# Performance work log

Measured on AMD Instinct MI355X. Metric: run time of the kernel, lower is better.

The kernel has to match this reference:

```python
import jax, jax.numpy as jnp
import numpy as np

NUM_HEADS = 8
Q_DIM = 32  # == k_dim == v_dim (required by the broadcasted matmul in the source)

def _conv1x1(x, w, b):
    # x: [B, C, H, W]; w: [O, C]; b: [O]  (1x1 conv == channel matmul)
    return jnp.einsum('bchw,oc->bohw', x, w) + b[None, :, None, None]

def setup_inputs() -> dict:
    key = jax.random.key(0)
    ks = jax.random.split(key, 7)
    B, C, H, W = 16, 256, 64, 64
    O = Q_DIM * NUM_HEADS  # 256
    s = 1.0 / np.sqrt(C)
    return {
        'x':  jax.random.normal(ks[0], (B, C, H, W), jnp.float32),
        'wq': jax.random.normal(ks[1], (O, C), jnp.float32) * s,
        'bq': jax.random.normal(ks[2], (O,), jnp.float32) * 0.01,
        'wk': jax.random.normal(ks[3], (O, C), jnp.float32) * s,
        'bk': jax.random.normal(ks[4], (O,), jnp.float32) * 0.01,
        'wv': jax.random.normal(ks[5], (O, C), jnp.float32) * s,
        'bv': jax.random.normal(ks[6], (O,), jnp.float32) * 0.01,
    }

def reference(x, wq, bq, wk, bk, wv, bv):
    B, C, H, W = x.shape
    nH, d = NUM_HEADS, Q_DIM
    q = _conv1x1(x, wq, bq).reshape(B, nH, d, H, W)
    k = _conv1x1(x, wk, bk).reshape(B, nH, d, H, W)
    v = _conv1x1(x, wv, bv).reshape(B, nH, d, H, W)
    # torch.matmul(q, k.transpose(-2,-1)): contract over width, batched over (B, nH, d)
    scores = jnp.einsum('bndhw,bndgw->bndhg', q, k) / jnp.sqrt(jnp.asarray(d, x.dtype))
    weights = jax.nn.softmax(scores, axis=-1)  # [B, nH, d, H, H]
    ctx = jnp.einsum('bndhg,bndgw->bndhw', weights, v)
    return ctx.reshape(B, nH * d, H, W)
```

## Files before the change

kernel.cpp:

```cpp
#include <hip/hip_runtime.h>
#include <stdint.h>

#define LOG2E       1.4426950408889634f
#define INV_SQRT32  0.17677669529663687f

using bf16x8 = __attribute__((ext_vector_type(8))) short;
using f32x4  = __attribute__((ext_vector_type(4))) float;

__device__ __forceinline__ unsigned short f2bf(float f) {
  union { float f; uint32_t u; } v; v.f = f;
  uint32_t r = v.u + 0x7fffu + ((v.u >> 16) & 1u);
  return (unsigned short)(r >> 16);
}

typedef const __attribute__((address_space(1))) void* gas_ptr;
typedef __attribute__((address_space(3))) void*       las_ptr;
__device__ __forceinline__ void load_lds16(const void* g, void* l) {
  __builtin_amdgcn_global_load_lds((gas_ptr)g, (las_ptr)l, 16, 0, 0);
}

__global__ __launch_bounds__(256) void convert_w(
    const float* __restrict__ wq, const float* __restrict__ bq,
    const float* __restrict__ wk, const float* __restrict__ bk,
    const float* __restrict__ wv, const float* __restrict__ bv,
    unsigned short* __restrict__ Wcat, float* __restrict__ biasc) {
  int idx = (blockIdx.x * 256 + threadIdx.x) * 4;
  int p = idx >> 16;
  int rem = idx & 0xffff;
  const float* src = (p == 0) ? wq : (p == 1) ? wk : wv;
  float4 v = *(const float4*)(src + rem);
  ushort4 o;
  o.x = f2bf(v.x); o.y = f2bf(v.y); o.z = f2bf(v.z); o.w = f2bf(v.w);
  *(ushort4*)(Wcat + idx) = o;
  if (blockIdx.x < 3) {
    const float* sb = (blockIdx.x == 0) ? bq : (blockIdx.x == 1) ? bk : bv;
    biasc[blockIdx.x * 256 + threadIdx.x] = sb[threadIdx.x];
  }
}

__global__ __launch_bounds__(256) void transpose_x(const float* __restrict__ x,
                                                   unsigned short* __restrict__ xt) {
  __shared__ float tile[64 * 65];
  int b = blockIdx.z;
  int s0 = blockIdx.x * 64, c0 = blockIdx.y * 64;
  int t = threadIdx.x;
  int sl = t & 63, g = t >> 6;
  const float* xp = x + ((size_t)(b * 256 + c0)) * 4096 + s0 + sl;
#pragma unroll
  for (int ii = 0; ii < 16; ++ii) {
    int cl = g * 16 + ii;
    tile[cl * 65 + sl] = xp[(size_t)cl * 4096];
  }
  __syncthreads();
#pragma unroll
  for (int jj = 0; jj < 16; ++jj) {
    int s_loc = g * 16 + jj;
    float v = tile[sl * 65 + s_loc];
    xt[((size_t)(b * 4096 + s0 + s_loc)) * 256 + c0 + sl] = f2bf(v);
  }
}

__global__ __launch_bounds__(256) void gemm_qkv(
    const unsigned short* __restrict__ Wc, const float* __restrict__ biasc,
    const unsigned short* __restrict__ Xt, unsigned short* __restrict__ qkv) {
  __shared__ unsigned short As[128 * 32];
  __shared__ unsigned short Bs[128 * 32];
  int blk = blockIdx.x;
  int b = blk / 192;
  int rest = blk - b * 192;
  int mt = rest >> 5, nt = rest & 31;
  int m0 = mt * 128, n0 = nt * 128;
  int tid = threadIdx.x;
  int lane = tid & 63, wave = tid >> 6;
  int quad = lane >> 4, rt = lane & 15;
  int wm = wave >> 1, wn = wave & 1;

  f32x4 acc[4][4];
#pragma unroll
  for (int i = 0; i < 4; ++i)
#pragma unroll
    for (int j = 0; j < 4; ++j) acc[i][j] = (f32x4){0.f, 0.f, 0.f, 0.f};

  int lr = lane >> 2;
  int lk = (lane & 3) * 8;
  const unsigned short* gA0 = Wc + (size_t)(m0 + (wave * 2 + 0) * 16 + lr) * 256 + lk;
  const unsigned short* gA1 = Wc + (size_t)(m0 + (wave * 2 + 1) * 16 + lr) * 256 + lk;
  const unsigned short* gB0 = Xt + ((size_t)b * 4096 + n0 + (wave * 2 + 0) * 16 + lr) * 256 + lk;
  const unsigned short* gB1 = Xt + ((size_t)b * 4096 + n0 + (wave * 2 + 1) * 16 + lr) * 256 + lk;
  unsigned short* lA0 = &As[(wave * 2 + 0) * 16 * 32];
  unsigned short* lA1 = &As[(wave * 2 + 1) * 16 * 32];
  unsigned short* lB0 = &Bs[(wave * 2 + 0) * 16 * 32];
  unsigned short* lB1 = &Bs[(wave * 2 + 1) * 16 * 32];

#pragma unroll
  for (int kc = 0; kc < 8; ++kc) {
    int ko = kc * 32;
    load_lds16(gA0 + ko, lA0);
    load_lds16(gA1 + ko, lA1);
    load_lds16(gB0 + ko, lB0);
    load_lds16(gB1 + ko, lB1);
    __syncthreads();
    bf16x8 af[4], bfr[4];
#pragma unroll
    for (int mi = 0; mi < 4; ++mi)
      af[mi] = *(const bf16x8*)&As[(wm * 64 + mi * 16 + rt) * 32 + quad * 8];
#pragma unroll
    for (int ni = 0; ni < 4; ++ni)
      bfr[ni] = *(const bf16x8*)&Bs[(wn * 64 + ni * 16 + rt) * 32 + quad * 8];
#pragma unroll
    for (int mi = 0; mi < 4; ++mi)
#pragma unroll
      for (int ni = 0; ni < 4; ++ni)
        acc[mi][ni] = __builtin_amdgcn_mfma_f32_16x16x32_bf16(af[mi], bfr[ni], acc[mi][ni], 0, 0, 0);
    __syncthreads();
  }

  size_t obase = (size_t)b * 768;
#pragma unroll
  for (int mi = 0; mi < 4; ++mi) {
    int o = m0 + wm * 64 + mi * 16 + quad * 4;
    float bsv[4];
#pragma unroll
    for (int r = 0; r < 4; ++r) bsv[r] = biasc[o + r];
#pragma unroll
    for (int ni = 0; ni < 4; ++ni) {
      int s = n0 + wn * 64 + ni * 16 + rt;
#pragma unroll
      for (int r = 0; r < 4; ++r)
        qkv[(obase + o + r) * 4096 + s] = f2bf(acc[mi][ni][r] + bsv[r]);
    }
  }
}

__global__ __launch_bounds__(256) void attn(const unsigned short* __restrict__ qkv,
                                            float* __restrict__ out) {
  __shared__ char sh[36608];
  unsigned short* Qs = (unsigned short*)sh;
  unsigned short* Ks = (unsigned short*)(sh + 9216);
  float*          Sf = (float*)sh;
  unsigned short* Ps = (unsigned short*)(sh + 16640);
  unsigned short* Vt = (unsigned short*)(sh + 25856);
  float* red    = (float*)(sh + 35072);
  float* rowmax = (float*)(sh + 36096);
  float* rowinv = (float*)(sh + 36352);

  int blk = blockIdx.x;
  int b = blk >> 8, o = blk & 255;
  int t = threadIdx.x;
  size_t base = ((size_t)b * 768 + o) * 4096;
  const unsigned short* qg = qkv + base;
  const unsigned short* kg = qkv + base + (size_t)256 * 4096;
  const unsigned short* vg = qkv + base + (size_t)512 * 4096;

  {
    int h = t >> 2, w0 = (t & 3) * 16;
    const uint4* qp = (const uint4*)(qg + h * 64 + w0);
    const uint4* kp = (const uint4*)(kg + h * 64 + w0);
    uint4 q0 = qp[0], q1 = qp[1];
    uint4 k0 = kp[0], k1 = kp[1];
    *(uint4*)&Qs[h * 72 + w0]     = q0;
    *(uint4*)&Qs[h * 72 + w0 + 8] = q1;
    *(uint4*)&Ks[h * 72 + w0]     = k0;
    *(uint4*)&Ks[h * 72 + w0 + 8] = k1;

    int w = t & 63, gb = (t >> 6) * 16;
    unsigned short vv[16];
#pragma unroll
    for (int j = 0; j < 16; ++j) vv[j] = vg[(size_t)(gb + j) * 64 + w];
    *(uint4*)&Vt[w * 72 + gb]     = ((uint4*)vv)[0];
    *(uint4*)&Vt[w * 72 + gb + 8] = ((uint4*)vv)[1];
  }
  __syncthreads();

  int lane = t & 63, wave = t >> 6;
  int rt = lane & 15, quad = lane >> 4;
  int wm = wave >> 1, wn = wave & 1;

  f32x4 accs[2][2];
#pragma unroll
  for (int i = 0; i < 2; ++i)
#pragma unroll
    for (int j = 0; j < 2; ++j) accs[i][j] = (f32x4){0.f, 0.f, 0.f, 0.f};
#pragma unroll
  for (int ks = 0; ks < 2; ++ks) {
    int kk = ks * 32 + quad * 8;
    bf16x8 a0 = *(const bf16x8*)&Qs[(wm * 32 + rt) * 72 + kk];
    bf16x8 a1 = *(const bf16x8*)&Qs[(wm * 32 + 16 + rt) * 72 + kk];
    bf16x8 b0 = *(const bf16x8*)&Ks[(wn * 32 + rt) * 72 + kk];
    bf16x8 b1 = *(const bf16x8*)&Ks[(wn * 32 + 16 + rt) * 72 + kk];
    accs[0][0] = __builtin_amdgcn_mfma_f32_16x16x32_bf16(a0, b0, accs[0][0], 0, 0, 0);
    accs[0][1] = __builtin_amdgcn_mfma_f32_16x16x32_bf16(a0, b1, accs[0][1], 0, 0, 0);
    accs[1][0] = __builtin_amdgcn_mfma_f32_16x16x32_bf16(a1, b0, accs[1][0], 0, 0, 0);
    accs[1][1] = __builtin_amdgcn_mfma_f32_16x16x32_bf16(a1, b1, accs[1][1], 0, 0, 0);
  }
  __syncthreads();

#pragma unroll
  for (int tm = 0; tm < 2; ++tm)
#pragma unroll
    for (int tn = 0; tn < 2; ++tn)
#pragma unroll
      for (int r = 0; r < 4; ++r)
        Sf[(wm * 32 + tm * 16 + quad * 4 + r) * 65 + wn * 32 + tn * 16 + rt] =
            accs[tm][tn][r] * INV_SQRT32;
  __syncthreads();

  int hr = t & 63, qt = t >> 6;
  float s[16];
#pragma unroll
  for (int e = 0; e < 16; ++e) s[e] = Sf[hr * 65 + qt * 16 + e];
  float m = s[0];
#pragma unroll
  for (int e = 1; e < 16; ++e) m = fmaxf(m, s[e]);
  red[qt * 64 + hr] = m;
  __syncthreads();
  if (t < 64)
    rowmax[t] = fmaxf(fmaxf(red[t], red[64 + t]), fmaxf(red[128 + t], red[192 + t]));
  __syncthreads();
  float mr = rowmax[hr];
  float ssum = 0.f;
  unsigned short pv[16];
#pragma unroll
  for (int e = 0; e < 16; ++e) {
    float p = exp2f((s[e] - mr) * LOG2E);
    ssum += p;
    pv[e] = f2bf(p);
  }
  *(uint4*)&Ps[hr * 72 + qt * 16]     = ((uint4*)pv)[0];
  *(uint4*)&Ps[hr * 72 + qt * 16 + 8] = ((uint4*)pv)[1];
  red[qt * 64 + hr] = ssum;
  __syncthreads();
  if (t < 64) rowinv[t] = 1.f / (red[t] + red[64 + t] + red[128 + t] + red[192 + t]);
  __syncthreads();

  f32x4 acco[2][2];
#pragma unroll
  for (int i = 0; i < 2; ++i)
#pragma unroll
    for (int j = 0; j < 2; ++j) acco[i][j] = (f32x4){0.f, 0.f, 0.f, 0.f};
#pragma unroll
  for (int ks = 0; ks < 2; ++ks) {
    int kk = ks * 32 + quad * 8;
    bf16x8 a0 = *(const bf16x8*)&Ps[(wm * 32 + rt) * 72 + kk];
    bf16x8 a1 = *(const bf16x8*)&Ps[(wm * 32 + 16 + rt) * 72 + kk];
    bf16x8 b0 = *(const bf16x8*)&Vt[(wn * 32 + rt) * 72 + kk];
    bf16x8 b1 = *(const bf16x8*)&Vt[(wn * 32 + 16 + rt) * 72 + kk];
    acco[0][0] = __builtin_amdgcn_mfma_f32_16x16x32_bf16(a0, b0, acco[0][0], 0, 0, 0);
    acco[0][1] = __builtin_amdgcn_mfma_f32_16x16x32_bf16(a0, b1, acco[0][1], 0, 0, 0);
    acco[1][0] = __builtin_amdgcn_mfma_f32_16x16x32_bf16(a1, b0, acco[1][0], 0, 0, 0);
    acco[1][1] = __builtin_amdgcn_mfma_f32_16x16x32_bf16(a1, b1, acco[1][1], 0, 0, 0);
  }

  float* op = out + ((size_t)(b * 256 + o)) * 4096;
#pragma unroll
  for (int tm = 0; tm < 2; ++tm) {
#pragma unroll
    for (int r = 0; r < 4; ++r) {
      int h = wm * 32 + tm * 16 + quad * 4 + r;
      float inv = rowinv[h];
#pragma unroll
      for (int tn = 0; tn < 2; ++tn) {
        int w = wn * 32 + tn * 16 + rt;
        op[h * 64 + w] = acco[tm][tn][r] * inv;
      }
    }
  }
}

extern "C" void kernel_launch(void* const* d_in, const int* in_sizes, int n_in,
                              void* d_out, int out_size, void* d_ws, size_t ws_size,
                              hipStream_t stream) {
  const float* x  = (const float*)d_in[0];
  const float* wq = (const float*)d_in[1];
  const float* bq = (const float*)d_in[2];
  const float* wk = (const float*)d_in[3];
  const float* bk = (const float*)d_in[4];
  const float* wv = (const float*)d_in[5];
  const float* bv = (const float*)d_in[6];
  float* out = (float*)d_out;

  char* ws = (char*)d_ws;
  unsigned short* Wcat  = (unsigned short*)ws;
  float*          biasc = (float*)(ws + 393216);
  unsigned short* Xt    = (unsigned short*)(ws + 396288);
  unsigned short* qkv   = (unsigned short*)(ws + 396288 + 33554432);

  hipLaunchKernelGGL(convert_w, dim3(192), dim3(256), 0, stream,
                     wq, bq, wk, bk, wv, bv, Wcat, biasc);
  hipLaunchKernelGGL(transpose_x, dim3(64, 4, 16), dim3(256), 0, stream, x, Xt);
  hipLaunchKernelGGL(gemm_qkv, dim3(3072), dim3(256), 0, stream, Wcat, biasc, Xt, qkv);
  hipLaunchKernelGGL(attn, dim3(4096), dim3(256), 0, stream, qkv, out);
}
```

Measured before the change: 199.4 us.

## Vectorize transpose stores and restage QKV GEMM with full-K smem tiles

The transpose kernel now packs eight bf16 values per thread and writes them with a single 16-byte store, replacing strided 2-byte scalar stores. The QKV GEMM moves from 128x128 tiles with per-K-chunk sync to 64x64 tiles that load the whole K=256 slab into shared memory at once. The loop then runs eight MFMA steps with no barriers in between. This removes seven barrier pairs and launches four times as many blocks, which should help occupancy. In exchange, each tile gets less operand reuse, global traffic for A and B rises, and each block uses 64KB of LDS.

```diff
diff --git a/kernel.cpp b/kernel.cpp
--- a/kernel.cpp
+++ b/kernel.cpp
@@ -52,82 +52,77 @@
     tile[cl * 65 + sl] = xp[(size_t)cl * 4096];
   }
   __syncthreads();
-#pragma unroll
-  for (int jj = 0; jj < 16; ++jj) {
-    int s_loc = g * 16 + jj;
-    float v = tile[sl * 65 + s_loc];
-    xt[((size_t)(b * 4096 + s0 + s_loc)) * 256 + c0 + sl] = f2bf(v);
+  int c8 = (t & 7) * 8;
+  int rbase = t >> 3;
+#pragma unroll
+  for (int half = 0; half < 2; ++half) {
+    int row = rbase + half * 32;
+    unsigned short p[8];
+#pragma unroll
+    for (int i = 0; i < 8; ++i) p[i] = f2bf(tile[(c8 + i) * 65 + row]);
+    *(uint4*)&xt[((size_t)(b * 4096 + s0 + row)) * 256 + c0 + c8] = *(uint4*)p;
   }
 }
 
 __global__ __launch_bounds__(256) void gemm_qkv(
     const unsigned short* __restrict__ Wc, const float* __restrict__ biasc,
     const unsigned short* __restrict__ Xt, unsigned short* __restrict__ qkv) {
-  __shared__ unsigned short As[128 * 32];
-  __shared__ unsigned short Bs[128 * 32];
-  int blk = blockIdx.x;
-  int b = blk / 192;
-  int rest = blk - b * 192;
-  int mt = rest >> 5, nt = rest & 31;
-  int m0 = mt * 128, n0 = nt * 128;
-  int tid = threadIdx.x;
-  int lane = tid & 63, wave = tid >> 6;
-  int quad = lane >> 4, rt = lane & 15;
-  int wm = wave >> 1, wn = wave & 1;
-
-  f32x4 acc[4][4];
-#pragma unroll
-  for (int i = 0; i < 4; ++i)
-#pragma unroll
-    for (int j = 0; j < 4; ++j) acc[i][j] = (f32x4){0.f, 0.f, 0.f, 0.f};
-
+  __shared__ unsigned short As[8 * 64 * 32];
+  __shared__ unsigned short Bs[8 * 64 * 32];
+  int nt = blockIdx.x, mt = blockIdx.y, b = blockIdx.z;
+  int m0 = mt * 64, n0 = nt * 64;
+  int t = threadIdx.x;
+  int lane = t & 63, wave = t >> 6;
   int lr = lane >> 2;
   int lk = (lane & 3) * 8;
-  const unsigned short* gA0 = Wc + (size_t)(m0 + (wave * 2 + 0) * 16 + lr) * 256 + lk;
-  const unsigned short* gA1 = Wc + (size_t)(m0 + (wave * 2 + 1) * 16 + lr) * 256 + lk;
-  const unsigned short* gB0 = Xt + ((size_t)b * 4096 + n0 + (wave * 2 + 0) * 16 + lr) * 256 + lk;
-  const unsigned short* gB1 = Xt + ((size_t)b * 4096 + n0 + (wave * 2 + 1) * 16 + lr) * 256 + lk;
-  unsigned short* lA0 = &As[(wave * 2 + 0) * 16 * 32];
-  unsigned short* lA1 = &As[(wave * 2 + 1) * 16 * 32];
-  unsigned short* lB0 = &Bs[(wave * 2 + 0) * 16 * 32];
-  unsigned short* lB1 = &Bs[(wave * 2 + 1) * 16 * 32];
+  const unsigned short* Abase = Wc + (size_t)m0 * 256;
+  const unsigned short* Bbase = Xt + ((size_t)b * 4096 + n0) * 256;
+
+#pragma unroll
+  for (int r4 = 0; r4 < 4; ++r4) {
+#pragma unroll
+    for (int cc = 0; cc < 2; ++cc) {
+      int kc = wave * 2 + cc;
+      load_lds16(Abase + (size_t)(r4 * 16 + lr) * 256 + kc * 32 + lk,
+                 &As[kc * 2048 + r4 * 512]);
+      load_lds16(Bbase + (size_t)(r4 * 16 + lr) * 256 + kc * 32 + lk,
+                 &Bs[kc * 2048 + r4 * 512]);
+    }
+  }
+  __syncthreads();
+
+  int rt = lane & 15, quad = lane >> 4;
+  int wm = wave >> 1, wn = wave & 1;
+  f32x4 acc[2][2];
+#pragma unroll
+  for (int i = 0; i < 2; ++i)
+#pragma unroll
+    for (int j = 0; j < 2; ++j) acc[i][j] = (f32x4){0.f, 0.f, 0.f, 0.f};
 
 #pragma unroll
   for (int kc = 0; kc < 8; ++kc) {
-    int ko = kc * 32;
-    load_lds16(gA0 + ko, lA0);
-    load_lds16(gA1 + ko, lA1);
-    load_lds16(gB0 + ko, lB0);
-    load_lds16(gB1 + ko, lB1);
-    __syncthreads();
-    bf16x8 af[4], bfr[4];
-#pragma unroll
-    for (int mi = 0; mi < 4; ++mi)
-      af[mi] = *(const bf16x8*)&As[(wm * 64 + mi * 16 + rt) * 32 + quad * 8];
-#pragma unroll
-    for (int ni = 0; ni < 4; ++ni)
-      bfr[ni] = *(const bf16x8*)&Bs[(wn * 64 + ni * 16 + rt) * 32 + quad * 8];
-#pragma unroll
-    for (int mi = 0; mi < 4; ++mi)
-#pragma unroll
-      for (int ni = 0; ni < 4; ++ni)
-        acc[mi][ni] = __builtin_amdgcn_mfma_f32_16x16x32_bf16(af[mi], bfr[ni], acc[mi][ni], 0, 0, 0);
-    __syncthreads();
+    bf16x8 a0 = *(const bf16x8*)&As[kc * 2048 + (wm * 32 + rt) * 32 + quad * 8];
+    bf16x8 a1 = *(const bf16x8*)&As[kc * 2048 + (wm * 32 + 16 + rt) * 32 + quad * 8];
+    bf16x8 b0 = *(const bf16x8*)&Bs[kc * 2048 + (wn * 32 + rt) * 32 + quad * 8];
+    bf16x8 b1 = *(const bf16x8*)&Bs[kc * 2048 + (wn * 32 + 16 + rt) * 32 + quad * 8];
+    acc[0][0] = __builtin_amdgcn_mfma_f32_16x16x32_bf16(a0, b0, acc[0][0], 0, 0, 0);
+    acc[0][1] = __builtin_amdgcn_mfma_f32_16x16x32_bf16(a0, b1, acc[0][1], 0, 0, 0);
+    acc[1][0] = __builtin_amdgcn_mfma_f32_16x16x32_bf16(a1, b0, acc[1][0], 0, 0, 0);
+    acc[1][1] = __builtin_amdgcn_mfma_f32_16x16x32_bf16(a1, b1, acc[1][1], 0, 0, 0);
   }
 
   size_t obase = (size_t)b * 768;
 #pragma unroll
-  for (int mi = 0; mi < 4; ++mi) {
-    int o = m0 + wm * 64 + mi * 16 + quad * 4;
-    float bsv[4];
-#pragma unroll
-    for (int r = 0; r < 4; ++r) bsv[r] = biasc[o + r];
-#pragma unroll
-    for (int ni = 0; ni < 4; ++ni) {
-      int s = n0 + wn * 64 + ni * 16 + rt;
-#pragma unroll
-      for (int r = 0; r < 4; ++r)
-        qkv[(obase + o + r) * 4096 + s] = f2bf(acc[mi][ni][r] + bsv[r]);
+  for (int mi = 0; mi < 2; ++mi) {
+    int orow = m0 + wm * 32 + mi * 16 + quad * 4;
+#pragma unroll
+    for (int r = 0; r < 4; ++r) {
+      float bv = biasc[orow + r];
+#pragma unroll
+      for (int ni = 0; ni < 2; ++ni) {
+        int s = n0 + wn * 32 + ni * 16 + rt;
+        qkv[(obase + orow + r) * 4096 + s] = f2bf(acc[mi][ni][r] + bv);
+      }
     }
   }
 }
@@ -288,6 +283,6 @@
   hipLaunchKernelGGL(convert_w, dim3(192), dim3(256), 0, stream,
                      wq, bq, wk, bk, wv, bv, Wcat, biasc);
   hipLaunchKernelGGL(transpose_x, dim3(64, 4, 16), dim3(256), 0, stream, x, Xt);
-  hipLaunchKernelGGL(gemm_qkv, dim3(3072), dim3(256), 0, stream, Wcat, biasc, Xt, qkv);
+  hipLaunchKernelGGL(gemm_qkv, dim3(64, 12, 16), dim3(256), 0, stream, Wcat, biasc, Xt, qkv);
   hipLaunchKernelGGL(attn, dim3(4096), dim3(256), 0, stream, qkv, out);
 }
```

New measurement: 213.5 us. 1.07x slower.
